# Optimization experiments

Hardware: AMD Instinct MI355X
Metric: run time of the kernel (lower is better)

Reference implementation:

```python
import jax, jax.numpy as jnp
import numpy as np

B, W, N = 64, 128, 64
EGC, EGL = 8, 12          # Graph_Constructor dim, GraphLearning embed dim
HID = 77                  # ceil(0.6 * window_size)
ET = 2 * N                # gatv2 doubles embed_dim (= n_features by default)
TOPK = 20
SLOPE = 0.2               # leaky relu alpha


def _batch_edges(e, batch, n):
    # replicate (2,E) edge list per batch element with node offset i*n
    off = (jnp.arange(batch, dtype=e.dtype) * n)[None, :, None]
    return (e[:, None, :] + off).reshape(2, -1)


def setup_inputs() -> dict:
    key = jax.random.key(0)
    ks = jax.random.split(key, 20)
    g = lambda i, shp, s=0.1: jax.random.normal(ks[i], shp, jnp.float32) * s
    p = {
        "x": jax.random.normal(ks[0], (B, W, N), jnp.float32),
        # Graph_Constructor (only used to build edges in preprocessing)
        "emb1": g(1, (N, EGC), 1.0), "emb2": g(2, (N, EGC), 1.0),
        "gc_w1": g(3, (EGC, EGC)), "gc_b1": jnp.zeros(EGC, jnp.float32),
        "gc_w2": g(4, (EGC, EGC)), "gc_b2": jnp.zeros(EGC, jnp.float32),
        # GraphLearning
        "gl_embed": g(5, (N, EGL), 1.0),
        "gcn_w": g(6, (W + EGL, W)), "gcn_b": jnp.zeros(W, jnp.float32),
        "mlp_w1": g(7, (W, HID)), "mlp_b1": jnp.zeros(HID, jnp.float32),
        "mlp_w2": g(8, (HID, W)), "mlp_b2": jnp.zeros(W, jnp.float32),
        # TemporalAttentionLayer (use_gatv2=True): lin: 2N -> ET, a: (ET,1)
        "ta_w": g(9, (2 * N, ET)), "ta_b": jnp.zeros(ET, jnp.float32),
        "ta_a": g(10, (ET,), 1.0), "ta_bias": jnp.zeros((W, W), jnp.float32),
        # GATConv(window, window)
        "gat_w": g(11, (W, W)), "gat_asrc": g(12, (W,), 1.0),
        "gat_adst": g(13, (W,), 1.0), "gat_b": jnp.zeros(W, jnp.float32),
        # forecasting head Linear(W,1)
        "fc_w": g(14, (W, 1)), "fc_b": jnp.zeros(1, jnp.float32),
    }
    # ---- Graph_Constructor edge preprocessing (top-20 neighbors/node) ----
    n1 = jnp.tanh(3.0 * (p["emb1"] @ p["gc_w1"] + p["gc_b1"]))
    n2 = jnp.tanh(3.0 * (p["emb2"] @ p["gc_w2"] + p["gc_b2"]))
    a = n1 @ n2.T - n2 @ n1.T
    adj = jax.nn.relu(jnp.tanh(3.0 * a))
    noise = jax.random.uniform(ks[15], (N, N), jnp.float32) * 0.01
    _, t1 = jax.lax.top_k(adj + noise, TOPK)            # (N, 20)
    rows = jnp.repeat(jnp.arange(N), TOPK)
    edges = jnp.stack([rows, t1.reshape(-1)]).astype(jnp.int32)
    # ---- GraphLearning cosine-similarity edges (keep N^2 - ceil(0.6 N^2)) ----
    wgt = p["gl_embed"]
    nrm = jnp.linalg.norm(wgt, axis=-1)
    cos = (wgt @ wgt.T) / (nrm[:, None] * nrm[None, :])
    n_keep = N * N - int(np.ceil(0.6 * N * N))          # 1638
    _, idx = jax.lax.top_k(cos.reshape(-1), n_keep)
    idx = jnp.sort(idx)                                  # coo row-major order
    gl_edges = jnp.stack([idx // N, idx % N]).astype(jnp.int32)
    p["batch_edge_index"] = _batch_edges(edges, B, N)        # (2, 20*N*B)
    p["gl_batch_edge_index"] = _batch_edges(gl_edges, B, N)  # (2, 1638*B)
    return p


def _gcn(x, ei, w, b, nseg):
    # GCNConv: self-loops + symmetric degree normalization
    src, dst = ei[0], ei[1]
    sl = jnp.arange(nseg, dtype=ei.dtype)
    src = jnp.concatenate([src, sl]); dst = jnp.concatenate([dst, sl])
    deg = jax.ops.segment_sum(jnp.ones(dst.shape, jnp.float32), dst, nseg)
    dinv = jax.lax.rsqrt(jnp.maximum(deg, 1.0))
    h = x @ w
    msg = h[src] * (dinv[src] * dinv[dst])[:, None]
    return jax.ops.segment_sum(msg, dst, nseg) + b


def _gat(x, ei, w, asrc, adst, b, nseg):
    # single-head GATConv with self-loops, softmax over incoming edges
    src, dst = ei[0], ei[1]
    sl = jnp.arange(nseg, dtype=ei.dtype)
    src = jnp.concatenate([src, sl]); dst = jnp.concatenate([dst, sl])
    h = x @ w
    e = jax.nn.leaky_relu(h[src] @ asrc + h[dst] @ adst, SLOPE)
    emax = jax.ops.segment_max(e, dst, nseg)
    ee = jnp.exp(e - emax[dst])
    denom = jax.ops.segment_sum(ee, dst, nseg)
    alpha = ee / denom[dst]
    return jax.ops.segment_sum(h[src] * alpha[:, None], dst, nseg) + b


def _temporal_attn(v, w, bl, a, bias):
    # GATv2-style: e[b,i,j] = a . leakyrelu(W [v_i || v_j] + bl) + bias[i,j]
    # split W to avoid materializing the (B,K,K,2N) concat tensor
    wi, wj = w[:N], w[N:]
    left = v @ wi            # (B,K,ET)
    right = v @ wj           # (B,K,ET)
    s = jax.nn.leaky_relu(left[:, :, None, :] + right[:, None, :, :] + bl, SLOPE)
    e = jnp.einsum('bije,e->bij', s, a) + bias          # (B,K,K)
    attn = jax.nn.softmax(e, axis=2)                    # dropout off (eval)
    return jnp.tanh(attn @ v)                           # (B,K,N)


def reference(x, emb1, emb2, gc_w1, gc_b1, gc_w2, gc_b2, gl_embed, gcn_w, gcn_b,
              mlp_w1, mlp_b1, mlp_w2, mlp_b2, ta_w, ta_b, ta_a, ta_bias,
              gat_w, gat_asrc, gat_adst, gat_b, fc_w, fc_b,
              batch_edge_index, gl_batch_edge_index):
    Bn = B * N
    xp = jnp.transpose(x, (0, 2, 1))                    # (B,N,W)
    x_batch = xp.reshape(Bn, W)
    # ---- GraphLearning: concat node embeddings, GCN, relu, tanh MLP ----
    all_emb = jnp.tile(gl_embed, (B, 1))                # (B*N, 12)
    h = _gcn(jnp.concatenate([x_batch, all_emb], 1), gl_batch_edge_index,
             gcn_w, gcn_b, Bn)
    h = jax.nn.relu(h)
    x_rec = jnp.tanh(jnp.tanh(h @ mlp_w1 + mlp_b1) @ mlp_w2 + mlp_b2)  # (B*N,W)
    # ---- residual + temporal attention over window dim ----
    xs = x_batch + x_rec
    v = jnp.transpose(xs.reshape(B, N, W), (0, 2, 1))   # (B,W,N)
    ht = _temporal_attn(v, ta_w, ta_b, ta_a, ta_bias)   # (B,W,N)
    # ---- feature GAT + forecasting head ----
    hg = jnp.transpose(ht, (0, 2, 1)).reshape(Bn, W)
    hg = _gat(hg, batch_edge_index, gat_w, gat_asrc, gat_adst, gat_b, Bn)
    x_pre = jnp.tanh(hg @ fc_w + fc_b).reshape(B, 1, N)
    out_rec = jnp.transpose(x_rec.reshape(B, N, W), (0, 2, 1))  # (B,W,N)
    return out_rec, x_pre
```

## Files before the change

kernel.cpp:

```cpp
#include <hip/hip_runtime.h>
#include <math.h>

#define BB  64
#define WW  128
#define NN  64
#define HIDN 77

__global__ __launch_bounds__(1024) void k_front(
    const float* __restrict__ x, const float* __restrict__ emb,
    const float* __restrict__ wg, const float* __restrict__ gcn_b,
    const float* __restrict__ w1, const float* __restrict__ b1,
    const float* __restrict__ w2, const float* __restrict__ b2,
    const int* __restrict__ gl_ei, int E_gl,
    const int* __restrict__ gat_ei, int E_gat,
    const float* __restrict__ gat_w, const float* __restrict__ asrc,
    const float* __restrict__ adst, const float* __restrict__ fcw,
    const float* __restrict__ gat_b,
    float* __restrict__ xs, float* __restrict__ out_rec,
    float* __restrict__ VAV, int* __restrict__ gat_off, int* __restrict__ gat_list) {
  __shared__ float smem[37312];
  float* Ws   = smem;
  float* W1s  = smem + 17920;
  float* XA   = smem + 28160;
  float* Sm   = smem + 30464;
  float* xbt  = smem + 31552;
  float* hm   = smem + 33664;
  float* recT = smem + 34944;
  float* gbb  = smem + 37120;
  int*   cnt  = (int*)(smem + 37248);
  float* scr4 = smem + 33664;
  float* scr6 = smem + 34944;

  int tid = threadIdx.x;

  if (blockIdx.x >= 256) {
    int which = blockIdx.x - 256;
    if (which < 3) {
      const float* vecg = (which == 0) ? asrc : (which == 1) ? adst : fcw;
      if (tid < 128) {
        float acc = 0.f;
#pragma unroll 4
        for (int k = 0; k < 128; k++) acc += gat_w[tid * 128 + k] * vecg[k];
        VAV[which * 128 + tid] = acc;
      }
      if (which == 2) {
        float* red = smem;
        if (tid < 128) red[tid] = gat_b[tid] * fcw[tid];
        __syncthreads();
        if (tid == 0) {
          float s = 0.f;
          for (int i = 0; i < 128; i++) s += red[i];
          VAV[384] = s;
        }
      }
    } else {
      int* ip   = (int*)smem;
      int* offs = ip;
      int* cur  = ip + 65;
      int* cntg = ip + 129;
      int* lst  = ip + 193;
      if (tid < 64) cntg[tid] = 1;
      __syncthreads();
      for (int e = tid; e < E_gat; e += 1024) atomicAdd(&cntg[gat_ei[BB * E_gat + e]], 1);
      __syncthreads();
      if (tid == 0) { int s = 0; for (int n = 0; n < 64; n++) { offs[n] = s; s += cntg[n]; } offs[64] = s; }
      __syncthreads();
      if (tid < 64) cur[tid] = offs[tid];
      __syncthreads();
      for (int e = tid; e < E_gat; e += 1024) {
        int src = gat_ei[e], dst = gat_ei[BB * E_gat + e];
        lst[atomicAdd(&cur[dst], 1)] = src;
      }
      if (tid < 64) lst[atomicAdd(&cur[tid], 1)] = tid;
      __syncthreads();
      if (tid < 65) gat_off[tid] = offs[tid];
      int tot = offs[64];
      for (int t = tid; t < tot; t += 1024) gat_list[t] = lst[t];
    }
    return;
  }

  int r0 = blockIdx.x * 16;
  int b = r0 >> 6, n0 = r0 & 63;
  const float* xb  = x + (size_t)b * 8192;
  const float* xb2 = xb + n0;

  {
    const float4* W4 = (const float4*)wg;
    float4* Ws4 = (float4*)Ws;
    for (int t = tid; t < 4480; t += 1024) Ws4[t] = W4[t];
  }
  for (int t = tid; t < 2048; t += 1024) {
    int w = t >> 4, i = t & 15;
    xbt[i * 132 + w] = xb2[w * 64 + i];
  }
  for (int t = tid; t < 1088; t += 1024) Sm[t] = 0.f;
  if (tid < 128) gbb[tid] = gcn_b[tid];
  if (tid < 64) cnt[tid] = 1;
  __syncthreads();

  for (int e = tid; e < E_gl; e += 1024) {
    int dst = gl_ei[BB * E_gl + e];
    atomicAdd(&cnt[dst], 1);
    int d = dst - n0;
    if ((unsigned)d < 16u) Sm[d * 68 + gl_ei[e]] = 1.0f;
  }
  __syncthreads();

  for (int t = tid; t < 1088; t += 1024) {
    int i = t / 68, s = t % 68;
    if (s < 64) {
      float di = rsqrtf((float)cnt[n0 + i]);
      float v = Sm[t] * rsqrtf((float)cnt[s]) * di;
      if (s == n0 + i) v += di * di;
      Sm[t] = v;
    }
  }
  __syncthreads();

  {
    int i = tid >> 6, tw = tid & 63;
    const float* Sr = Sm + i * 68;
    float o0 = 0, o1 = 0;
#pragma unroll 4
    for (int s4 = 0; s4 < 16; s4++) {
      float4 sv = *(const float4*)&Sr[s4 * 4];
      float4 x0 = *(const float4*)&xb[tw * 64 + s4 * 4];
      float4 x1 = *(const float4*)&xb[(tw + 64) * 64 + s4 * 4];
      o0 += sv.x * x0.x + sv.y * x0.y + sv.z * x0.z + sv.w * x0.w;
      o1 += sv.x * x1.x + sv.y * x1.y + sv.z * x1.z + sv.w * x1.w;
    }
    float* Xr = XA + i * 144;
    Xr[tw] = o0; Xr[tw + 64] = o1;
  }
  if (tid < 192) {
    int i = tid / 12, j = tid % 12;
    const float* Sr = Sm + i * 68;
    float a = 0.f;
    for (int s = 0; s < 64; s++) a += Sr[s] * emb[s * 12 + j];
    XA[i * 144 + 128 + j] = a;
  }
  __syncthreads();

  {
    int half = tid >> 9, t = tid & 511;
    int row = t >> 5, cg = t & 31;
    int c0 = cg * 4;
    float a0 = 0, a1 = 0, a2 = 0, a3 = 0;
    const float* Ar = XA + row * 144;
    int k0 = half * 70;
#pragma unroll 5
    for (int k = k0; k < k0 + 70; k++) {
      float4 wv = *(const float4*)&Ws[k * 128 + c0];
      float a = Ar[k];
      a0 += a * wv.x; a1 += a * wv.y; a2 += a * wv.z; a3 += a * wv.w;
    }
    if (half) *(float4*)&scr4[t * 4] = make_float4(a0, a1, a2, a3);
    __syncthreads();
    if (!half) {
      float4 p = *(const float4*)&scr4[t * 4];
      float4 bv = *(const float4*)&gbb[c0];
      *(float4*)&XA[row * 144 + c0] = make_float4(
          fmaxf(a0 + p.x + bv.x, 0.f), fmaxf(a1 + p.y + bv.y, 0.f),
          fmaxf(a2 + p.z + bv.z, 0.f), fmaxf(a3 + p.w + bv.w, 0.f));
    }
    for (int q = tid; q < 10240; q += 1024) {
      int k = q / 80, c = q % 80;
      W1s[q] = (c < HIDN) ? w1[k * HIDN + c] : 0.f;
    }
  }
  __syncthreads();

  {
    bool act = tid < 640;
    int half6 = (tid >= 320) ? 1 : 0;
    int s = act ? (half6 ? tid - 320 : tid) : 0;
    int rp = s / 20, cg = s % 20;
    int c0 = cg * 4;
    float a0 = 0, a1 = 0, a2 = 0, a3 = 0;
    if (act) {
      const float* Ar = XA + rp * 144;
      int k0 = half6 * 64;
#pragma unroll 4
      for (int k = k0; k < k0 + 64; k++) {
        float4 wv = *(const float4*)&W1s[k * 80 + c0];
        float a = Ar[k];
        a0 += a * wv.x; a1 += a * wv.y; a2 += a * wv.z; a3 += a * wv.w;
      }
      if (half6) *(float4*)&scr6[s * 4] = make_float4(a0, a1, a2, a3);
    }
    __syncthreads();
    if (act && !half6) {
      float4 p = *(const float4*)&scr6[s * 4];
      float rv[4] = {a0 + p.x, a1 + p.y, a2 + p.z, a3 + p.w};
#pragma unroll
      for (int j = 0; j < 4; j++) {
        int c = c0 + j;
        float bb = (c < HIDN) ? b1[c] : 0.f;
        hm[rp * 80 + c] = tanhf(rv[j] + bb);
      }
    }
  }
  __syncthreads();
  {
    const float4* w24 = (const float4*)w2;
    float4* Wb4 = (float4*)smem;
    for (int t = tid; t < 2464; t += 1024) Wb4[t] = w24[t];
  }
  __syncthreads();

  {
    if (tid < 512) {
      int row = tid >> 5, cg = tid & 31;
      int c0 = cg * 4;
      float a0 = 0, a1 = 0, a2 = 0, a3 = 0;
      const float* Hr = hm + row * 80;
#pragma unroll 4
      for (int k = 0; k < HIDN; k++) {
        float4 wv = *(const float4*)&smem[k * 128 + c0];
        float a = Hr[k];
        a0 += a * wv.x; a1 += a * wv.y; a2 += a * wv.z; a3 += a * wv.w;
      }
      float4 bv = *(const float4*)&b2[c0];
      float x0 = tanhf(a0 + bv.x), x1 = tanhf(a1 + bv.y);
      float x2 = tanhf(a2 + bv.z), x3 = tanhf(a3 + bv.w);
      const float* X0 = xbt + row * 132;
      *(float4*)&xs[(size_t)(r0 + row) * 128 + c0] =
          make_float4(X0[c0] + x0, X0[c0 + 1] + x1, X0[c0 + 2] + x2, X0[c0 + 3] + x3);
      recT[(c0 + 0) * 17 + row] = x0; recT[(c0 + 1) * 17 + row] = x1;
      recT[(c0 + 2) * 17 + row] = x2; recT[(c0 + 3) * 17 + row] = x3;
    }
  }
  __syncthreads();
  float* orc = out_rec + (size_t)b * 8192 + n0;
  for (int t = tid; t < 2048; t += 1024) {
    int w = t >> 4, i = t & 15;
    orc[w * 64 + i] = recT[w * 17 + i];
  }
}

__global__ __launch_bounds__(512) void k_attn(const float* __restrict__ xs, const float* __restrict__ ta_w,
                                              const float* __restrict__ ta_b, const float* __restrict__ ta_a,
                                              const float* __restrict__ ta_bias, const float* __restrict__ VAV,
                                              float* __restrict__ PART) {
  __shared__ float smem[38272];
  float* Rf  = smem;
  float* XN  = smem + 16384;
  float* WT  = smem + 25088;
  float* Lh  = smem + 33408;
  float* av2 = smem + 37632;
  float* av6 = smem + 37760;
  float* tbs = smem + 37888;
  float* uu  = smem + 38016;
  float* vv  = smem + 38048;
  float* vva = smem + 38176;
  float* vvd = smem + 38208;
  float* vvf = smem + 38240;
  float* scratch = WT;

  int tid = threadIdx.x;
  int b = blockIdx.x >> 2, q = blockIdx.x & 3;
  int i0 = q * 32;

  {
    const float* xsb = xs + (size_t)b * 8192;
#pragma unroll
    for (int t = 0; t < 16; t++) {
      int idx = tid + t * 512;
      XN[(idx >> 7) * 136 + (idx & 127)] = xsb[idx];
    }
  }
#pragma unroll
  for (int t = 0; t < 16; t++) {
    int idx = tid + t * 512;
    int e = idx & 127, n = idx >> 7;
    WT[e * 65 + n] = ta_w[(64 + n) * 128 + e];
  }
  if (tid < 128) {
    float a = ta_a[tid];
    av2[tid] = 0.4f * a; av6[tid] = 0.6f * a;
    tbs[tid] = ta_b[tid];
  }
  if (tid >= 128 && tid < 160) {
    int i = tid - 128;
    vva[i] = VAV[i0 + i];
    vvd[i] = VAV[128 + i0 + i];
    vvf[i] = VAV[256 + i0 + i];
  }
  __syncthreads();

  {
    int et = tid >> 4, jt = tid & 15;
    int e0 = et * 4, j0 = jt * 8;
    float acc[4][8];
#pragma unroll
    for (int r = 0; r < 4; r++)
#pragma unroll
      for (int c = 0; c < 8; c++) acc[r][c] = 0.f;
#pragma unroll 4
    for (int n = 0; n < 64; n++) {
      float4 b0 = *(const float4*)&XN[n * 136 + j0];
      float4 b1 = *(const float4*)&XN[n * 136 + j0 + 4];
      float bb[8] = {b0.x, b0.y, b0.z, b0.w, b1.x, b1.y, b1.z, b1.w};
#pragma unroll
      for (int r = 0; r < 4; r++) {
        float a = WT[(e0 + r) * 65 + n];
#pragma unroll
        for (int c = 0; c < 8; c++) acc[r][c] += a * bb[c];
      }
    }
#pragma unroll
    for (int r = 0; r < 4; r++) {
      *(float4*)&Rf[(e0 + r) * 128 + j0] = make_float4(acc[r][0], acc[r][1], acc[r][2], acc[r][3]);
      *(float4*)&Rf[(e0 + r) * 128 + j0 + 4] = make_float4(acc[r][4], acc[r][5], acc[r][6], acc[r][7]);
    }
  }
  __syncthreads();
#pragma unroll
  for (int t = 0; t < 16; t++) {
    int idx = tid + t * 512;
    int e = idx & 127, n = idx >> 7;
    WT[e * 65 + n] = ta_w[n * 128 + e];
  }
  __syncthreads();

  {
    int e = tid >> 2, ig = tid & 3;
    int ii = ig * 8;
    float acc[8];
#pragma unroll
    for (int c = 0; c < 8; c++) acc[c] = 0.f;
#pragma unroll 4
    for (int n = 0; n < 64; n++) {
      float4 b0 = *(const float4*)&XN[n * 136 + i0 + ii];
      float4 b1 = *(const float4*)&XN[n * 136 + i0 + ii + 4];
      float a = WT[e * 65 + n];
      acc[0] += a * b0.x; acc[1] += a * b0.y; acc[2] += a * b0.z; acc[3] += a * b0.w;
      acc[4] += a * b1.x; acc[5] += a * b1.y; acc[6] += a * b1.z; acc[7] += a * b1.w;
    }
    float tb = tbs[e];
#pragma unroll
    for (int c = 0; c < 8; c++) Lh[e * 32 + ii + c] = acc[c] + tb;
  }
  __syncthreads();

  if (tid < 160) {
    float acc = 0.f;
    if (tid < 128) {
      for (int e = 0; e < 128; e++) acc += av6[e] * Rf[e * 128 + tid];
      vv[tid] = acc;
    } else {
      int i = tid - 128;
      for (int e = 0; e < 128; e++) acc += av6[e] * Lh[e * 32 + i];
      uu[i] = acc;
    }
  }
  __syncthreads();

  bool act = tid < 256;
  int tj = tid & 31, ti = (tid >> 5) & 7;
  float p[4][4];
  if (act) {
    float acc[4][4];
#pragma unroll
    for (int a = 0; a < 4; a++)
#pragma unroll
      for (int j = 0; j < 4; j++) acc[a][j] = 0.f;
#pragma unroll 2
    for (int e = 0; e < 128; e++) {
      float4 Lv = *(const float4*)&Lh[e * 32 + ti * 4];
      float4 Rv = *(const float4*)&Rf[e * 128 + tj * 4];
      float ae = av2[e];
      float La[4] = {Lv.x, Lv.y, Lv.z, Lv.w};
      float Ra[4] = {Rv.x, Rv.y, Rv.z, Rv.w};
#pragma unroll
      for (int a = 0; a < 4; a++)
#pragma unroll
        for (int j = 0; j < 4; j++) {
          float t = La[a] + Ra[j];
          acc[a][j] += ae * fabsf(t);
        }
    }
#pragma unroll
    for (int a = 0; a < 4; a++) {
      int i = i0 + ti * 4 + a;
      float uvi = uu[ti * 4 + a];
      float4 bv = *(const float4*)&ta_bias[(size_t)i * 128 + tj * 4];
      float v0 = acc[a][0] + bv.x + uvi + vv[tj * 4 + 0];
      float v1 = acc[a][1] + bv.y + uvi + vv[tj * 4 + 1];
      float v2 = acc[a][2] + bv.z + uvi + vv[tj * 4 + 2];
      float v3 = acc[a][3] + bv.w + uvi + vv[tj * 4 + 3];
      float m = fmaxf(fmaxf(v0, v1), fmaxf(v2, v3));
#pragma unroll
      for (int o = 16; o > 0; o >>= 1) m = fmaxf(m, __shfl_xor(m, o));
      float e0 = __expf(v0 - m), e1 = __expf(v1 - m), e2 = __expf(v2 - m), e3 = __expf(v3 - m);
      float s = e0 + e1 + e2 + e3;
#pragma unroll
      for (int o = 16; o > 0; o >>= 1) s += __shfl_xor(s, o);
      float inv = 1.f / s;
      p[a][0] = e0 * inv; p[a][1] = e1 * inv; p[a][2] = e2 * inv; p[a][3] = e3 * inv;
    }
  }
  __syncthreads();
  float* P = Lh;
  if (act) {
#pragma unroll
    for (int a = 0; a < 4; a++)
      *(float4*)&P[(ti * 4 + a) * 132 + tj * 4] = make_float4(p[a][0], p[a][1], p[a][2], p[a][3]);
  }
  __syncthreads();

  int tn = tid & 15, i2 = tid >> 4;
  float o0 = 0, o1 = 0, o2 = 0, o3 = 0;
  const float* Prow = P + i2 * 132;
  const float* X0 = XN + (tn +  0) * 136;
  const float* X1 = XN + (tn + 16) * 136;
  const float* X2 = XN + (tn + 32) * 136;
  const float* X3 = XN + (tn + 48) * 136;
#pragma unroll 4
  for (int j4 = 0; j4 < 32; j4++) {
    float4 pv = *(const float4*)&Prow[j4 * 4];
    float4 a0 = *(const float4*)&X0[j4 * 4];
    float4 a1 = *(const float4*)&X1[j4 * 4];
    float4 a2 = *(const float4*)&X2[j4 * 4];
    float4 a3 = *(const float4*)&X3[j4 * 4];
    o0 += pv.x * a0.x + pv.y * a0.y + pv.z * a0.z + pv.w * a0.w;
    o1 += pv.x * a1.x + pv.y * a1.y + pv.z * a1.z + pv.w * a1.w;
    o2 += pv.x * a2.x + pv.y * a2.y + pv.z * a2.z + pv.w * a2.w;
    o3 += pv.x * a3.x + pv.y * a3.y + pv.z * a3.z + pv.w * a3.w;
  }
  float t0 = tanhf(o0), t1 = tanhf(o1), t2 = tanhf(o2), t3 = tanhf(o3);
  {
    float wa = vva[i2], wd = vvd[i2], wf = vvf[i2];
    int base = i2 * 66 + tn;
    scratch[base +  0] = t0 * wa; scratch[base + 16] = t1 * wa;
    scratch[base + 32] = t2 * wa; scratch[base + 48] = t3 * wa;
    scratch[2112 + base +  0] = t0 * wd; scratch[2112 + base + 16] = t1 * wd;
    scratch[2112 + base + 32] = t2 * wd; scratch[2112 + base + 48] = t3 * wd;
    scratch[4224 + base +  0] = t0 * wf; scratch[4224 + base + 16] = t1 * wf;
    scratch[4224 + base + 32] = t2 * wf; scratch[4224 + base + 48] = t3 * wf;
  }
  __syncthreads();
  if (tid < 192) {
    int arr = tid >> 6, n = tid & 63;
    const float* sp = scratch + arr * 2112 + n;
    float s = 0.f;
#pragma unroll 8
    for (int i = 0; i < 32; i++) s += sp[i * 66];
    PART[(size_t)b * 768 + q * 192 + arr * 64 + n] = s;
  }
}

__global__ __launch_bounds__(64) void k_fin(const float* __restrict__ PART, const float* __restrict__ VAV,
                                            const int* __restrict__ off, const int* __restrict__ list,
                                            const float* __restrict__ fcb, float* __restrict__ outp) {
  __shared__ float ss_s[64], sd_s[64], pf_s[64];
  int tid = threadIdx.x, b = blockIdx.x;
  const float* pb = PART + (size_t)b * 768;
  {
    float s0 = 0, s1 = 0, s2 = 0;
#pragma unroll
    for (int q2 = 0; q2 < 4; q2++) {
      const float* p = pb + q2 * 192;
      s0 += p[tid]; s1 += p[64 + tid]; s2 += p[128 + tid];
    }
    ss_s[tid] = s0; sd_s[tid] = s1; pf_s[tid] = s2;
  }
  __syncthreads();
  int e0 = off[tid], e1 = off[tid + 1];
  float sdv = sd_s[tid];
  float mx = -1e30f;
  for (int e = e0; e < e1; e++) {
    float t = ss_s[list[e]] + sdv;
    t = fmaxf(t, 0.2f * t);
    mx = fmaxf(mx, t);
  }
  float den = 0.f, acc = 0.f;
  for (int e = e0; e < e1; e++) {
    int s = list[e];
    float t = ss_s[s] + sdv;
    t = fmaxf(t, 0.2f * t);
    float w = __expf(t - mx);
    den += w;
    acc += w * pf_s[s];
  }
  outp[b * 64 + tid] = tanhf(acc / den + VAV[384] + fcb[0]);
}

extern "C" void kernel_launch(void* const* d_in, const int* in_sizes, int n_in,
                              void* d_out, int out_size, void* d_ws, size_t ws_size,
                              hipStream_t stream) {
  (void)n_in; (void)out_size; (void)ws_size;
  const float* x        = (const float*)d_in[0];
  const float* gl_embed = (const float*)d_in[7];
  const float* gcn_w    = (const float*)d_in[8];
  const float* gcn_b    = (const float*)d_in[9];
  const float* mlp_w1   = (const float*)d_in[10];
  const float* mlp_b1   = (const float*)d_in[11];
  const float* mlp_w2   = (const float*)d_in[12];
  const float* mlp_b2   = (const float*)d_in[13];
  const float* ta_w     = (const float*)d_in[14];
  const float* ta_b     = (const float*)d_in[15];
  const float* ta_a     = (const float*)d_in[16];
  const float* ta_bias  = (const float*)d_in[17];
  const float* gat_w    = (const float*)d_in[18];
  const float* gat_asrc = (const float*)d_in[19];
  const float* gat_adst = (const float*)d_in[20];
  const float* gat_b    = (const float*)d_in[21];
  const float* fc_w     = (const float*)d_in[22];
  const float* fc_b     = (const float*)d_in[23];
  const int*   gat_ei   = (const int*)d_in[24];
  const int*   gl_ei    = (const int*)d_in[25];

  int E_gat = in_sizes[24] / (2 * BB);
  int E_gl  = in_sizes[25] / (2 * BB);

  float* ws = (float*)d_ws;
  float* XS    = ws + 0;
  int*   IP    = (int*)(ws + 524288);
  int* GATOFF  = IP;
  int* GATLIST = IP + 72;
  float* VAV   = ws + 526848;
  float* PART  = ws + 527360;

  float* out_rec = (float*)d_out;
  float* out_pre = (float*)d_out + 524288;

  k_front<<<260, 1024, 0, stream>>>(x, gl_embed, gcn_w, gcn_b, mlp_w1, mlp_b1, mlp_w2, mlp_b2,
                                    gl_ei, E_gl, gat_ei, E_gat,
                                    gat_w, gat_asrc, gat_adst, fc_w, gat_b,
                                    XS, out_rec, VAV, GATOFF, GATLIST);
  k_attn<<<256, 512, 0, stream>>>(XS, ta_w, ta_b, ta_a, ta_bias, VAV, PART);
  k_fin<<<64, 64, 0, stream>>>(PART, VAV, GATOFF, GATLIST, fc_b, out_pre);
}
```

Baseline: 78.51 us.

## Halve k_front tile to 8 rows with 512 threads and smaller LDS footprint

k_front now processes 8 node rows per block with 512 threads instead of 16 rows with 1024 threads, launching 516 blocks instead of 260. The split-K partial sums and scratch buffers are removed, W1 reuses the Ws region, and the transposed x staging buffer is dropped in favour of direct global reads for the residual. LDS use falls from about 149KB to about 82KB, which is meant to allow more blocks in flight on more CUs. In exchange the gcn_w and mlp weight matrices are loaded from global memory twice as often, and each thread accumulates two outputs with float2 loads instead of four with float4.

```diff
diff --git a/kernel.cpp b/kernel.cpp
--- a/kernel.cpp
+++ b/kernel.cpp
@@ -6,7 +6,7 @@
 #define NN  64
 #define HIDN 77
 
-__global__ __launch_bounds__(1024) void k_front(
+__global__ __launch_bounds__(512) void k_front(
     const float* __restrict__ x, const float* __restrict__ emb,
     const float* __restrict__ wg, const float* __restrict__ gcn_b,
     const float* __restrict__ w1, const float* __restrict__ b1,
@@ -18,23 +18,19 @@
     const float* __restrict__ gat_b,
     float* __restrict__ xs, float* __restrict__ out_rec,
     float* __restrict__ VAV, int* __restrict__ gat_off, int* __restrict__ gat_list) {
-  __shared__ float smem[37312];
+  __shared__ float smem[20448];
   float* Ws   = smem;
-  float* W1s  = smem + 17920;
-  float* XA   = smem + 28160;
-  float* Sm   = smem + 30464;
-  float* xbt  = smem + 31552;
-  float* hm   = smem + 33664;
-  float* recT = smem + 34944;
-  float* gbb  = smem + 37120;
-  int*   cnt  = (int*)(smem + 37248);
-  float* scr4 = smem + 33664;
-  float* scr6 = smem + 34944;
+  float* XA   = smem + 17920;
+  float* Sm   = smem + 19072;
+  float* hm   = smem + 19616;
+  float* gbb  = smem + 20256;
+  int*   cnt  = (int*)(smem + 20384);
+  float* recT = smem + 17920;
 
   int tid = threadIdx.x;
 
-  if (blockIdx.x >= 256) {
-    int which = blockIdx.x - 256;
+  if (blockIdx.x >= 512) {
+    int which = blockIdx.x - 512;
     if (which < 3) {
       const float* vecg = (which == 0) ? asrc : (which == 1) ? adst : fcw;
       if (tid < 128) {
@@ -61,13 +57,13 @@
       int* lst  = ip + 193;
       if (tid < 64) cntg[tid] = 1;
       __syncthreads();
-      for (int e = tid; e < E_gat; e += 1024) atomicAdd(&cntg[gat_ei[BB * E_gat + e]], 1);
+      for (int e = tid; e < E_gat; e += 512) atomicAdd(&cntg[gat_ei[BB * E_gat + e]], 1);
       __syncthreads();
       if (tid == 0) { int s = 0; for (int n = 0; n < 64; n++) { offs[n] = s; s += cntg[n]; } offs[64] = s; }
       __syncthreads();
       if (tid < 64) cur[tid] = offs[tid];
       __syncthreads();
-      for (int e = tid; e < E_gat; e += 1024) {
+      for (int e = tid; e < E_gat; e += 512) {
         int src = gat_ei[e], dst = gat_ei[BB * E_gat + e];
         lst[atomicAdd(&cur[dst], 1)] = src;
       }
@@ -75,39 +71,34 @@
       __syncthreads();
       if (tid < 65) gat_off[tid] = offs[tid];
       int tot = offs[64];
-      for (int t = tid; t < tot; t += 1024) gat_list[t] = lst[t];
+      for (int t = tid; t < tot; t += 512) gat_list[t] = lst[t];
     }
     return;
   }
 
-  int r0 = blockIdx.x * 16;
+  int r0 = blockIdx.x * 8;
   int b = r0 >> 6, n0 = r0 & 63;
-  const float* xb  = x + (size_t)b * 8192;
-  const float* xb2 = xb + n0;
+  const float* xb = x + (size_t)b * 8192;
 
   {
     const float4* W4 = (const float4*)wg;
     float4* Ws4 = (float4*)Ws;
-    for (int t = tid; t < 4480; t += 1024) Ws4[t] = W4[t];
-  }
-  for (int t = tid; t < 2048; t += 1024) {
-    int w = t >> 4, i = t & 15;
-    xbt[i * 132 + w] = xb2[w * 64 + i];
-  }
-  for (int t = tid; t < 1088; t += 1024) Sm[t] = 0.f;
+    for (int t = tid; t < 4480; t += 512) Ws4[t] = W4[t];
+  }
+  for (int t = tid; t < 544; t += 512) Sm[t] = 0.f;
   if (tid < 128) gbb[tid] = gcn_b[tid];
   if (tid < 64) cnt[tid] = 1;
   __syncthreads();
 
-  for (int e = tid; e < E_gl; e += 1024) {
+  for (int e = tid; e < E_gl; e += 512) {
     int dst = gl_ei[BB * E_gl + e];
     atomicAdd(&cnt[dst], 1);
     int d = dst - n0;
-    if ((unsigned)d < 16u) Sm[d * 68 + gl_ei[e]] = 1.0f;
-  }
-  __syncthreads();
-
-  for (int t = tid; t < 1088; t += 1024) {
+    if ((unsigned)d < 8u) Sm[d * 68 + gl_ei[e]] = 1.0f;
+  }
+  __syncthreads();
+
+  for (int t = tid; t < 544; t += 512) {
     int i = t / 68, s = t % 68;
     if (s < 64) {
       float di = rsqrtf((float)cnt[n0 + i]);
@@ -133,7 +124,7 @@
     float* Xr = XA + i * 144;
     Xr[tw] = o0; Xr[tw + 64] = o1;
   }
-  if (tid < 192) {
+  if (tid < 96) {
     int i = tid / 12, j = tid % 12;
     const float* Sr = Sm + i * 68;
     float a = 0.f;
@@ -143,99 +134,79 @@
   __syncthreads();
 
   {
-    int half = tid >> 9, t = tid & 511;
-    int row = t >> 5, cg = t & 31;
-    int c0 = cg * 4;
-    float a0 = 0, a1 = 0, a2 = 0, a3 = 0;
+    int row = tid >> 6, cg = tid & 63;
+    int c0 = cg * 2;
+    float a0 = 0, a1 = 0;
     const float* Ar = XA + row * 144;
-    int k0 = half * 70;
-#pragma unroll 5
-    for (int k = k0; k < k0 + 70; k++) {
-      float4 wv = *(const float4*)&Ws[k * 128 + c0];
+#pragma unroll 4
+    for (int k = 0; k < 140; k++) {
+      float2 wv = *(const float2*)&Ws[k * 128 + c0];
       float a = Ar[k];
-      a0 += a * wv.x; a1 += a * wv.y; a2 += a * wv.z; a3 += a * wv.w;
-    }
-    if (half) *(float4*)&scr4[t * 4] = make_float4(a0, a1, a2, a3);
+      a0 += a * wv.x; a1 += a * wv.y;
+    }
     __syncthreads();
-    if (!half) {
-      float4 p = *(const float4*)&scr4[t * 4];
-      float4 bv = *(const float4*)&gbb[c0];
-      *(float4*)&XA[row * 144 + c0] = make_float4(
-          fmaxf(a0 + p.x + bv.x, 0.f), fmaxf(a1 + p.y + bv.y, 0.f),
-          fmaxf(a2 + p.z + bv.z, 0.f), fmaxf(a3 + p.w + bv.w, 0.f));
-    }
-    for (int q = tid; q < 10240; q += 1024) {
+    float2 bv = *(const float2*)&gbb[c0];
+    XA[row * 144 + c0]     = fmaxf(a0 + bv.x, 0.f);
+    XA[row * 144 + c0 + 1] = fmaxf(a1 + bv.y, 0.f);
+    for (int q = tid; q < 10240; q += 512) {
       int k = q / 80, c = q % 80;
-      W1s[q] = (c < HIDN) ? w1[k * HIDN + c] : 0.f;
-    }
-  }
-  __syncthreads();
-
-  {
-    bool act = tid < 640;
-    int half6 = (tid >= 320) ? 1 : 0;
-    int s = act ? (half6 ? tid - 320 : tid) : 0;
-    int rp = s / 20, cg = s % 20;
-    int c0 = cg * 4;
-    float a0 = 0, a1 = 0, a2 = 0, a3 = 0;
+      Ws[q] = (c < HIDN) ? w1[k * HIDN + c] : 0.f;
+    }
+  }
+  __syncthreads();
+
+  {
+    bool act = tid < 320;
     if (act) {
+      int rp = tid / 40, cg = tid % 40;
+      int c0 = cg * 2;
+      float a0 = 0, a1 = 0;
       const float* Ar = XA + rp * 144;
-      int k0 = half6 * 64;
-#pragma unroll 4
-      for (int k = k0; k < k0 + 64; k++) {
-        float4 wv = *(const float4*)&W1s[k * 80 + c0];
+#pragma unroll 4
+      for (int k = 0; k < 128; k++) {
+        float2 wv = *(const float2*)&Ws[k * 80 + c0];
         float a = Ar[k];
-        a0 += a * wv.x; a1 += a * wv.y; a2 += a * wv.z; a3 += a * wv.w;
+        a0 += a * wv.x; a1 += a * wv.y;
       }
-      if (half6) *(float4*)&scr6[s * 4] = make_float4(a0, a1, a2, a3);
-    }
-    __syncthreads();
-    if (act && !half6) {
-      float4 p = *(const float4*)&scr6[s * 4];
-      float rv[4] = {a0 + p.x, a1 + p.y, a2 + p.z, a3 + p.w};
-#pragma unroll
-      for (int j = 0; j < 4; j++) {
-        int c = c0 + j;
-        float bb = (c < HIDN) ? b1[c] : 0.f;
-        hm[rp * 80 + c] = tanhf(rv[j] + bb);
-      }
+      float b0 = (c0 < HIDN) ? b1[c0] : 0.f;
+      float b1v = (c0 + 1 < HIDN) ? b1[c0 + 1] : 0.f;
+      hm[rp * 80 + c0]     = tanhf(a0 + b0);
+      hm[rp * 80 + c0 + 1] = tanhf(a1 + b1v);
     }
   }
   __syncthreads();
   {
     const float4* w24 = (const float4*)w2;
     float4* Wb4 = (float4*)smem;
-    for (int t = tid; t < 2464; t += 1024) Wb4[t] = w24[t];
-  }
-  __syncthreads();
-
-  {
-    if (tid < 512) {
-      int row = tid >> 5, cg = tid & 31;
-      int c0 = cg * 4;
-      float a0 = 0, a1 = 0, a2 = 0, a3 = 0;
-      const float* Hr = hm + row * 80;
-#pragma unroll 4
-      for (int k = 0; k < HIDN; k++) {
-        float4 wv = *(const float4*)&smem[k * 128 + c0];
-        float a = Hr[k];
-        a0 += a * wv.x; a1 += a * wv.y; a2 += a * wv.z; a3 += a * wv.w;
-      }
-      float4 bv = *(const float4*)&b2[c0];
-      float x0 = tanhf(a0 + bv.x), x1 = tanhf(a1 + bv.y);
-      float x2 = tanhf(a2 + bv.z), x3 = tanhf(a3 + bv.w);
-      const float* X0 = xbt + row * 132;
-      *(float4*)&xs[(size_t)(r0 + row) * 128 + c0] =
-          make_float4(X0[c0] + x0, X0[c0 + 1] + x1, X0[c0 + 2] + x2, X0[c0 + 3] + x3);
-      recT[(c0 + 0) * 17 + row] = x0; recT[(c0 + 1) * 17 + row] = x1;
-      recT[(c0 + 2) * 17 + row] = x2; recT[(c0 + 3) * 17 + row] = x3;
-    }
+    for (int t = tid; t < 2464; t += 512) Wb4[t] = w24[t];
+  }
+  __syncthreads();
+
+  {
+    int row = tid >> 6, cg = tid & 63;
+    int c0 = cg * 2;
+    float a0 = 0, a1 = 0;
+    const float* Hr = hm + row * 80;
+#pragma unroll 4
+    for (int k = 0; k < HIDN; k++) {
+      float2 wv = *(const float2*)&smem[k * 128 + c0];
+      float a = Hr[k];
+      a0 += a * wv.x; a1 += a * wv.y;
+    }
+    float x0 = tanhf(a0 + b2[c0]);
+    float x1 = tanhf(a1 + b2[c0 + 1]);
+    int nn = n0 + row;
+    float s0 = x0 + xb[c0 * 64 + nn];
+    float s1 = x1 + xb[(c0 + 1) * 64 + nn];
+    *(float2*)&xs[(size_t)(r0 + row) * 128 + c0] = make_float2(s0, s1);
+    recT[c0 * 9 + row] = x0;
+    recT[(c0 + 1) * 9 + row] = x1;
   }
   __syncthreads();
   float* orc = out_rec + (size_t)b * 8192 + n0;
-  for (int t = tid; t < 2048; t += 1024) {
-    int w = t >> 4, i = t & 15;
-    orc[w * 64 + i] = recT[w * 17 + i];
+  for (int t = tid; t < 1024; t += 512) {
+    int w = t >> 3, i = t & 7;
+    orc[w * 64 + i] = recT[w * 9 + i];
   }
 }
 
@@ -526,10 +497,10 @@
   float* out_rec = (float*)d_out;
   float* out_pre = (float*)d_out + 524288;
 
-  k_front<<<260, 1024, 0, stream>>>(x, gl_embed, gcn_w, gcn_b, mlp_w1, mlp_b1, mlp_w2, mlp_b2,
-                                    gl_ei, E_gl, gat_ei, E_gat,
-                                    gat_w, gat_asrc, gat_adst, fc_w, gat_b,
-                                    XS, out_rec, VAV, GATOFF, GATLIST);
+  k_front<<<516, 512, 0, stream>>>(x, gl_embed, gcn_w, gcn_b, mlp_w1, mlp_b1, mlp_w2, mlp_b2,
+                                   gl_ei, E_gl, gat_ei, E_gat,
+                                   gat_w, gat_asrc, gat_adst, fc_w, gat_b,
+                                   XS, out_rec, VAV, GATOFF, GATLIST);
   k_attn<<<256, 512, 0, stream>>>(XS, ta_w, ta_b, ta_a, ta_bias, VAV, PART);
   k_fin<<<64, 64, 0, stream>>>(PART, VAV, GATOFF, GATLIST, fc_b, out_pre);
 }
```

Result: slower. 80.56 us (+2.6%).
